# Optimization experiments

Hardware: AMD Instinct MI355X
Metric: run time of the kernel (lower is better)

The kernel has to match this reference:

```python
import jax, jax.numpy as jnp
import numpy as np

BS, C_IN, C_OUT, K, STYLE_DIM, BANK = 8, 64, 64, 3, 512, 4
D = H = W = 32
EPS = 1e-8
STRIDE = 1
PAD = 1


def setup_inputs() -> dict:
    key = jax.random.key(0)
    ks = jax.random.split(key, 7)
    lim_f = 1.0 / np.sqrt(STYLE_DIM)
    return {
        "x": jax.random.normal(ks[0], (BS, C_IN, D, H, W), dtype=jnp.float32),
        "w": jax.random.normal(ks[1], (BS, STYLE_DIM), dtype=jnp.float32),
        "filter_w": jax.random.uniform(ks[2], (BANK, STYLE_DIM), jnp.float32, -lim_f, lim_f),
        "filter_b": jax.random.uniform(ks[3], (BANK,), jnp.float32, -lim_f, lim_f),
        "mod_w": jax.random.uniform(ks[4], (C_IN, STYLE_DIM), jnp.float32, -lim_f, lim_f),
        "mod_b": jax.random.uniform(ks[5], (C_IN,), jnp.float32, -lim_f, lim_f),
        "bank": jax.random.normal(ks[6], (BANK, C_OUT, C_IN, K, K, K), dtype=jnp.float32),
    }


def reference(x, w, filter_w, filter_b, mod_w, mod_b, bank):
    bs, c_in, d, h, ww = x.shape
    # bank selection weights: softmax over bank axis
    fwt = jax.nn.softmax(w @ filter_w.T + filter_b, axis=-1)          # [bs, bank]
    # per-sample weights from bank (bank layout: n, out, in, k, k, k)
    weighted = jnp.einsum('bn,noijkl->boijkl', fwt, bank)             # [bs, out, in, k, k, k]
    # style modulation over input channels
    mod = (w @ mod_w.T + mod_b).reshape(bs, 1, c_in, 1, 1, 1)
    mw = weighted * mod
    # demodulation: normalize each (sample, out-channel) filter
    demod = jax.lax.rsqrt(jnp.sum(mw * mw, axis=(2, 3, 4, 5), keepdims=True) + EPS)
    mw = mw * demod
    # grouped conv with groups = bs
    mw = mw.reshape(bs * C_OUT, c_in, K, K, K)
    xr = x.reshape(1, bs * c_in, d, h, ww)
    out = jax.lax.conv_general_dilated(
        xr, mw,
        window_strides=(STRIDE,) * 3,
        padding=[(PAD, PAD)] * 3,
        dimension_numbers=('NCDHW', 'OIDHW', 'NCDHW'),
        feature_group_count=bs,
    )
    return out.reshape(bs, C_OUT, out.shape[-3], out.shape[-2], out.shape[-1])
```

## Files before the change

### kernel.cpp

```cpp
#include <hip/hip_runtime.h>
#include <math.h>

#define BS 8
#define CIN 64
#define COUT 64
#define SDIM 512
#define NBANK 4
#define DSZ 32
#define SPATIAL (DSZ*DSZ*DSZ)
#define NTAP 27
#define CH 8
#define NCH 8
#define NKS 7
#define SLABTEX (1124*33)
#define WINTEX 3301
#define A2PERB 14336
#define XP_TEXELS (64*SLABTEX)
constexpr float EPS = 1e-8f;

typedef short bf16x8 __attribute__((ext_vector_type(8)));
typedef float f32x4 __attribute__((ext_vector_type(4)));

__device__ __forceinline__ unsigned pack2(float a, float b) {
    unsigned ua = __float_as_uint(a);
    unsigned ub = __float_as_uint(b);
    ua = (ua + 0x7fffu + ((ua >> 16) & 1u)) >> 16;
    ub = (ub + 0x7fffu + ((ub >> 16) & 1u)) & 0xffff0000u;
    return ua | ub;
}
__device__ __forceinline__ unsigned short bf16r(float f) {
    unsigned u = __float_as_uint(f);
    u = (u + 0x7fffu + ((u >> 16) & 1u)) >> 16;
    return (unsigned short)u;
}
__device__ __forceinline__ void gload_lds16(const int4* g, int4* l) {
    __builtin_amdgcn_global_load_lds(
        (const __attribute__((address_space(1))) unsigned int*)(const void*)g,
        (__attribute__((address_space(3))) unsigned int*)(void*)l, 16, 0, 0);
}

__global__ __launch_bounds__(256) void prep_fused(
        const float* __restrict__ x,
        const float* __restrict__ w,
        const float* __restrict__ filter_w,
        const float* __restrict__ filter_b,
        const float* __restrict__ mod_w,
        const float* __restrict__ mod_b,
        const float* __restrict__ bank,
        int4* __restrict__ xP,
        unsigned short* __restrict__ wA2) {
    const int gid = blockIdx.x;
    const int t   = threadIdx.x;

    if (gid < 128) {
        const int b   = gid >> 4;
        const int oc  = (gid & 15) * 4 + (t >> 6);
        const int ic  = t & 63;
        const float* wb = w + b * SDIM;

        float fw[NBANK];
#pragma unroll
        for (int n = 0; n < NBANK; ++n) {
            float p = 0.0f;
            const float* fr = filter_w + n * SDIM;
#pragma unroll
            for (int k = 0; k < 8; ++k) p += wb[ic + 64 * k] * fr[ic + 64 * k];
#pragma unroll
            for (int off = 32; off >= 1; off >>= 1) p += __shfl_xor(p, off, 64);
            fw[n] = p + filter_b[n];
        }
        float mx = fmaxf(fmaxf(fw[0], fw[1]), fmaxf(fw[2], fw[3]));
        float se = 0.0f;
#pragma unroll
        for (int n = 0; n < NBANK; ++n) { fw[n] = expf(fw[n] - mx); se += fw[n]; }
        const float inv = 1.0f / se;
        const float f0 = fw[0] * inv, f1 = fw[1] * inv, f2 = fw[2] * inv, f3 = fw[3] * inv;

        float m = mod_b[ic];
        {
            const float4* wv4 = (const float4*)wb;
            const float4* mr4 = (const float4*)(mod_w + ic * SDIM);
            for (int j = 0; j < SDIM / 4; ++j) {
                float4 a = wv4[j], c = mr4[j];
                m += a.x * c.x + a.y * c.y + a.z * c.z + a.w * c.w;
            }
        }

        const float* b0 = bank + (size_t)((0 * COUT + oc) * CIN + ic) * NTAP;
        const float* b1 = bank + (size_t)((1 * COUT + oc) * CIN + ic) * NTAP;
        const float* b2 = bank + (size_t)((2 * COUT + oc) * CIN + ic) * NTAP;
        const float* b3 = bank + (size_t)((3 * COUT + oc) * CIN + ic) * NTAP;

        float v[NTAP];
        float ss = 0.0f;
#pragma unroll
        for (int k = 0; k < NTAP; ++k) {
            float tv = f0 * b0[k] + f1 * b1[k] + f2 * b2[k] + f3 * b3[k];
            tv *= m;
            v[k] = tv;
            ss += tv * tv;
        }
#pragma unroll
        for (int off = 32; off >= 1; off >>= 1) ss += __shfl_xor(ss, off, 64);
        const float d = rsqrtf(ss + EPS);

        const int c_  = ic >> 3, icl = ic & 7;
        const int at_ = oc >> 4, ln_ = oc & 15;
        const size_t tb = (size_t)b * A2PERB + (size_t)at_ * 64 + ln_;
#pragma unroll
        for (int k = 0; k < 28; ++k) {
            const float val = (k < NTAP) ? v[k] * d : 0.0f;
            const size_t tex = tb + (size_t)(c_ * NKS + (k >> 2)) * 256 + (size_t)(k & 3) * 16;
            wA2[tex * 8 + icl] = bf16r(val);
        }
    } else {
        const int j2   = gid - 128;
        const int zidx = j2 % 34;
        const int ch   = (j2 / 34) & 7;
        const int b    = j2 / 272;
        int4* slab = xP + (size_t)(b * NCH + ch) * SLABTEX;
        const int4 z4 = make_int4(0, 0, 0, 0);

        if (zidx >= 32) {
            const int base = (zidx == 32) ? 0 : 1090 * 33;
            for (int p = t; p < 34 * 33; p += 256) slab[base + p] = z4;
            return;
        }
        const float* xc = x + ((size_t)b * CIN + ch * CH) * SPATIAL + zidx * 1024;
        int4* dst = slab + (34 + 33 * zidx) * 33;
        for (int p = t; p < 33 * 33; p += 256) {
            const int r  = p / 33;
            const int cx = p - r * 33;
            int4 vv = z4;
            if (r < 32 && cx > 0) {
                const float* s = xc + r * 32 + (cx - 1);
                vv.x = (int)pack2(s[0 * SPATIAL], s[1 * SPATIAL]);
                vv.y = (int)pack2(s[2 * SPATIAL], s[3 * SPATIAL]);
                vv.z = (int)pack2(s[4 * SPATIAL], s[5 * SPATIAL]);
                vv.w = (int)pack2(s[6 * SPATIAL], s[7 * SPATIAL]);
            }
            dst[p] = vv;
        }
    }
}

__global__ __launch_bounds__(512, 2) void conv3d_mfma(
        const int4* __restrict__ xP,
        const int4* __restrict__ wA2,
        float* __restrict__ out) {
    const int bid = blockIdx.x;
    const int b = bid & 7, z = bid >> 3;
    const int t  = threadIdx.x;
    const int ln = t & 15;
    const int hi = (t >> 4) & 3;
    const int wv = t >> 6;
    const int lane = t & 63;

    __shared__ int4 xs[2 * WINTEX];

    int offB[NKS];
#pragma unroll
    for (int ks = 0; ks < NKS; ++ks) {
        int tap = ks * 4 + hi;
        if (tap > 26) tap = 0;
        const int dz = tap / 9, r = tap - dz * 9, dy = r / 3, dx = r - dy * 3;
        offB[ks] = (dz * 1089 + dy * 33 + dx) * 16;
    }
    int baseB[8];
#pragma unroll
    for (int st = 0; st < 8; ++st)
        baseB[st] = ((wv * 4 + (st >> 1)) * 33 + (st & 1) * 16 + ln) * 16;

    auto stageX = [&](int c, int buf) {
        const int4* src = xP + (size_t)(b * NCH + c) * SLABTEX + (size_t)z * 1089;
        int4* dst = xs + buf * WINTEX;
#pragma unroll
        for (int i = 0; i < 7; ++i) {
            const int p = i * 512 + t;
            if (p < WINTEX)
                gload_lds16(src + p, dst + (p & ~63));
        }
    };

    const int4* wab = wA2 + (size_t)b * A2PERB;
    auto loadA = [&](int kk, bf16x8* dstf) {
        const int kkc = kk > 55 ? 55 : kk;
        const int4* p = wab + (size_t)kkc * 256 + lane;
#pragma unroll
        for (int at = 0; at < 4; ++at) {
            const int4 vv = p[at * 64];
            dstf[at] = *(const bf16x8*)&vv;
        }
    };

    f32x4 acc[4][8];
#pragma unroll
    for (int i = 0; i < 4; ++i)
#pragma unroll
        for (int j = 0; j < 8; ++j) acc[i][j] = (f32x4){0.f, 0.f, 0.f, 0.f};

    bf16x8 af0[4], af1[4];

    stageX(0, 0);
    loadA(0, af0);
    loadA(1, af1);
    __syncthreads();

    auto bodyc = [&](int c, bf16x8 (&S0)[4], bf16x8 (&S1)[4]) {
        if (c + 1 < NCH) stageX(c + 1, (c + 1) & 1);
        const char* Xb = (const char*)(xs + (c & 1) * WINTEX);
#pragma unroll
        for (int ks = 0; ks < NKS; ++ks) {
            bf16x8* cur = (ks & 1) ? S1 : S0;
            bf16x8 bf[8];
#pragma unroll
            for (int st = 0; st < 8; ++st)
                bf[st] = *(const bf16x8*)(Xb + baseB[st] + offB[ks]);
#pragma unroll
            for (int at = 0; at < 4; ++at)
#pragma unroll
                for (int st = 0; st < 8; ++st)
                    acc[at][st] = __builtin_amdgcn_mfma_f32_16x16x32_bf16(
                        cur[at], bf[st], acc[at][st], 0, 0, 0);
            loadA(c * NKS + ks + 2, cur);
        }
        __syncthreads();
    };

    for (int cp = 0; cp < 4; ++cp) {
        bodyc(2 * cp,     af0, af1);
        bodyc(2 * cp + 1, af1, af0);
    }

    float* ob = out + (size_t)b * COUT * SPATIAL + (size_t)z * 1024;
#pragma unroll
    for (int at = 0; at < 4; ++at) {
        const int oc = at * 16 + hi * 4;
#pragma unroll
        for (int st = 0; st < 8; ++st) {
            const int sp = (wv * 4 + (st >> 1)) * 32 + (st & 1) * 16 + ln;
#pragma unroll
            for (int r = 0; r < 4; ++r)
                ob[(size_t)(oc + r) * SPATIAL + sp] = acc[at][st][r];
        }
    }
}

extern "C" void kernel_launch(void* const* d_in, const int* in_sizes, int n_in,
                              void* d_out, int out_size, void* d_ws, size_t ws_size,
                              hipStream_t stream) {
    const float* x        = (const float*)d_in[0];
    const float* w        = (const float*)d_in[1];
    const float* filter_w = (const float*)d_in[2];
    const float* filter_b = (const float*)d_in[3];
    const float* mod_w    = (const float*)d_in[4];
    const float* mod_b    = (const float*)d_in[5];
    const float* bank     = (const float*)d_in[6];
    float* out = (float*)d_out;

    int4* xP = (int4*)d_ws;
    unsigned short* wA2 = (unsigned short*)(xP + XP_TEXELS);

    prep_fused<<<128 + 34 * 8 * 8, 256, 0, stream>>>(
        x, w, filter_w, filter_b, mod_w, mod_b, bank, xP, wA2);
    conv3d_mfma<<<256, 512, 0, stream>>>(xP, (const int4*)wA2, out);
}
```

Measured before the change: 96.79 us.

## Switch conv to 32x32x16 MFMA with weights staged in shared memory

The implicit-GEMM conv moves from 16x16x32 to 32x32x16 bf16 MFMA tiles, with each MFMA now covering two taps of 8 channels. The weight tensor is re-laid out in the prep kernel to match. Weights are now double-buffered in LDS through global_load_lds alongside the input window, instead of being loaded from global into registers each step. s_setprio is raised around the MFMA bursts. The aim is fewer B-fragment LDS reads per MFMA and less global weight traffic, at the cost of more LDS per block and a different accumulator layout.

```diff
diff --git a/kernel.cpp b/kernel.cpp
--- a/kernel.cpp
+++ b/kernel.cpp
@@ -11,15 +11,17 @@
 #define NTAP 27
 #define CH 8
 #define NCH 8
-#define NKS 7
+#define NST 14
 #define SLABTEX (1124*33)
 #define WINTEX 3301
-#define A2PERB 14336
+#define XBUFT 3304
+#define ABUFT 1792
+#define A3PERB (NCH*NST*128)
 #define XP_TEXELS (64*SLABTEX)
 constexpr float EPS = 1e-8f;
 
 typedef short bf16x8 __attribute__((ext_vector_type(8)));
-typedef float f32x4 __attribute__((ext_vector_type(4)));
+typedef float f32x16 __attribute__((ext_vector_type(16)));
 
 __device__ __forceinline__ unsigned pack2(float a, float b) {
     unsigned ua = __float_as_uint(a);
@@ -48,7 +50,7 @@
         const float* __restrict__ mod_b,
         const float* __restrict__ bank,
         int4* __restrict__ xP,
-        unsigned short* __restrict__ wA2) {
+        unsigned short* __restrict__ wA3) {
     const int gid = blockIdx.x;
     const int t   = threadIdx.x;
 
@@ -105,13 +107,13 @@
         const float d = rsqrtf(ss + EPS);
 
         const int c_  = ic >> 3, icl = ic & 7;
-        const int at_ = oc >> 4, ln_ = oc & 15;
-        const size_t tb = (size_t)b * A2PERB + (size_t)at_ * 64 + ln_;
+        const int at_ = oc >> 5, ln_ = oc & 31;
 #pragma unroll
         for (int k = 0; k < 28; ++k) {
             const float val = (k < NTAP) ? v[k] * d : 0.0f;
-            const size_t tex = tb + (size_t)(c_ * NKS + (k >> 2)) * 256 + (size_t)(k & 3) * 16;
-            wA2[tex * 8 + icl] = bf16r(val);
+            const size_t tex = ((size_t)(b * NCH + c_) * NST + (k >> 1)) * 128
+                             + (size_t)at_ * 64 + (size_t)(k & 1) * 32 + ln_;
+            wA3[tex * 8 + icl] = bf16r(val);
         }
     } else {
         const int j2   = gid - 128;
@@ -146,104 +148,97 @@
 
 __global__ __launch_bounds__(512, 2) void conv3d_mfma(
         const int4* __restrict__ xP,
-        const int4* __restrict__ wA2,
+        const int4* __restrict__ wA3,
         float* __restrict__ out) {
     const int bid = blockIdx.x;
     const int b = bid & 7, z = bid >> 3;
-    const int t  = threadIdx.x;
-    const int ln = t & 15;
-    const int hi = (t >> 4) & 3;
-    const int wv = t >> 6;
-    const int lane = t & 63;
-
-    __shared__ int4 xs[2 * WINTEX];
-
-    int offB[NKS];
-#pragma unroll
-    for (int ks = 0; ks < NKS; ++ks) {
-        int tap = ks * 4 + hi;
+    const int t    = threadIdx.x;
+    const int l    = t & 63;
+    const int ln31 = t & 31;
+    const int h2   = (t >> 5) & 1;
+    const int wv   = t >> 6;
+
+    __shared__ int4 smem[2 * XBUFT + 2 * ABUFT];
+
+    int offB[NST];
+#pragma unroll
+    for (int s = 0; s < NST; ++s) {
+        int tap = 2 * s + h2;
         if (tap > 26) tap = 0;
         const int dz = tap / 9, r = tap - dz * 9, dy = r / 3, dx = r - dy * 3;
-        offB[ks] = (dz * 1089 + dy * 33 + dx) * 16;
+        offB[s] = (dz * 1089 + dy * 33 + dx) * 16;
     }
-    int baseB[8];
-#pragma unroll
-    for (int st = 0; st < 8; ++st)
-        baseB[st] = ((wv * 4 + (st >> 1)) * 33 + (st & 1) * 16 + ln) * 16;
-
-    auto stageX = [&](int c, int buf) {
-        const int4* src = xP + (size_t)(b * NCH + c) * SLABTEX + (size_t)z * 1089;
-        int4* dst = xs + buf * WINTEX;
+    int baseB[4];
+#pragma unroll
+    for (int st = 0; st < 4; ++st)
+        baseB[st] = ((wv * 4 + st) * 33 + ln31) * 16;
+
+    auto stage = [&](int c, int buf) {
+        const int4* xsrc = xP + (size_t)(b * NCH + c) * SLABTEX + (size_t)z * 1089;
+        const int4* asrc = wA3 + (size_t)(b * NCH + c) * ABUFT;
+        int4* lx = smem + buf * XBUFT;
+        int4* la = smem + 2 * XBUFT + buf * ABUFT;
 #pragma unroll
         for (int i = 0; i < 7; ++i) {
             const int p = i * 512 + t;
-            if (p < WINTEX)
-                gload_lds16(src + p, dst + (p & ~63));
+            if (p < WINTEX) gload_lds16(xsrc + p, lx + (p & ~63));
+        }
+#pragma unroll
+        for (int i = 0; i < 4; ++i) {
+            const int p = i * 512 + t;
+            if (p < ABUFT) gload_lds16(asrc + p, la + (p & ~63));
         }
     };
 
-    const int4* wab = wA2 + (size_t)b * A2PERB;
-    auto loadA = [&](int kk, bf16x8* dstf) {
-        const int kkc = kk > 55 ? 55 : kk;
-        const int4* p = wab + (size_t)kkc * 256 + lane;
-#pragma unroll
-        for (int at = 0; at < 4; ++at) {
-            const int4 vv = p[at * 64];
-            dstf[at] = *(const bf16x8*)&vv;
-        }
-    };
-
-    f32x4 acc[4][8];
-#pragma unroll
-    for (int i = 0; i < 4; ++i)
-#pragma unroll
-        for (int j = 0; j < 8; ++j) acc[i][j] = (f32x4){0.f, 0.f, 0.f, 0.f};
-
-    bf16x8 af0[4], af1[4];
-
-    stageX(0, 0);
-    loadA(0, af0);
-    loadA(1, af1);
+    f32x16 acc[2][4];
+#pragma unroll
+    for (int i = 0; i < 2; ++i)
+#pragma unroll
+        for (int j = 0; j < 4; ++j)
+#pragma unroll
+            for (int r = 0; r < 16; ++r) acc[i][j][r] = 0.0f;
+
+    stage(0, 0);
     __syncthreads();
 
-    auto bodyc = [&](int c, bf16x8 (&S0)[4], bf16x8 (&S1)[4]) {
-        if (c + 1 < NCH) stageX(c + 1, (c + 1) & 1);
-        const char* Xb = (const char*)(xs + (c & 1) * WINTEX);
-#pragma unroll
-        for (int ks = 0; ks < NKS; ++ks) {
-            bf16x8* cur = (ks & 1) ? S1 : S0;
-            bf16x8 bf[8];
-#pragma unroll
-            for (int st = 0; st < 8; ++st)
-                bf[st] = *(const bf16x8*)(Xb + baseB[st] + offB[ks]);
-#pragma unroll
-            for (int at = 0; at < 4; ++at)
-#pragma unroll
-                for (int st = 0; st < 8; ++st)
-                    acc[at][st] = __builtin_amdgcn_mfma_f32_16x16x32_bf16(
-                        cur[at], bf[st], acc[at][st], 0, 0, 0);
-            loadA(c * NKS + ks + 2, cur);
+    for (int c = 0; c < NCH; ++c) {
+        if (c + 1 < NCH) stage(c + 1, (c + 1) & 1);
+        const char* Xb = (const char*)(smem + (c & 1) * XBUFT);
+        const char* Ab = (const char*)(smem + 2 * XBUFT + (c & 1) * ABUFT);
+#pragma unroll
+        for (int s = 0; s < NST; ++s) {
+            bf16x8 a[2];
+#pragma unroll
+            for (int at = 0; at < 2; ++at)
+                a[at] = *(const bf16x8*)(Ab + s * 2048 + at * 1024 + l * 16);
+            bf16x8 bfr[4];
+#pragma unroll
+            for (int st = 0; st < 4; ++st)
+                bfr[st] = *(const bf16x8*)(Xb + baseB[st] + offB[s]);
+            __builtin_amdgcn_s_setprio(1);
+#pragma unroll
+            for (int at = 0; at < 2; ++at)
+#pragma unroll
+                for (int st = 0; st < 4; ++st)
+                    acc[at][st] = __builtin_amdgcn_mfma_f32_32x32x16_bf16(
+                        a[at], bfr[st], acc[at][st], 0, 0, 0);
+            __builtin_amdgcn_s_setprio(0);
         }
         __syncthreads();
-    };
-
-    for (int cp = 0; cp < 4; ++cp) {
-        bodyc(2 * cp,     af0, af1);
-        bodyc(2 * cp + 1, af1, af0);
     }
 
     float* ob = out + (size_t)b * COUT * SPATIAL + (size_t)z * 1024;
 #pragma unroll
-    for (int at = 0; at < 4; ++at) {
-        const int oc = at * 16 + hi * 4;
-#pragma unroll
-        for (int st = 0; st < 8; ++st) {
-            const int sp = (wv * 4 + (st >> 1)) * 32 + (st & 1) * 16 + ln;
-#pragma unroll
-            for (int r = 0; r < 4; ++r)
-                ob[(size_t)(oc + r) * SPATIAL + sp] = acc[at][st][r];
-        }
-    }
+    for (int at = 0; at < 2; ++at)
+#pragma unroll
+        for (int st = 0; st < 4; ++st) {
+            const int sp = (wv * 4 + st) * 32 + ln31;
+#pragma unroll
+            for (int r = 0; r < 16; ++r) {
+                const int oc = at * 32 + (r & 3) + 8 * (r >> 2) + 4 * h2;
+                ob[(size_t)oc * SPATIAL + sp] = acc[at][st][r];
+            }
+        }
 }
 
 extern "C" void kernel_launch(void* const* d_in, const int* in_sizes, int n_in,
@@ -259,9 +254,9 @@
     float* out = (float*)d_out;
 
     int4* xP = (int4*)d_ws;
-    unsigned short* wA2 = (unsigned short*)(xP + XP_TEXELS);
+    unsigned short* wA3 = (unsigned short*)(xP + XP_TEXELS);
 
     prep_fused<<<128 + 34 * 8 * 8, 256, 0, stream>>>(
-        x, w, filter_w, filter_b, mod_w, mod_b, bank, xP, wA2);
-    conv3d_mfma<<<256, 512, 0, stream>>>(xP, (const int4*)wA2, out);
-}
+        x, w, filter_w, filter_b, mod_w, mod_b, bank, xP, wA3);
+    conv3d_mfma<<<256, 512, 0, stream>>>(xP, (const int4*)wA3, out);
+}
```

Measured after the change: 86.58 us. -10.6%, faster.
